# Optimization experiments

Hardware: AMD Instinct MI355X
Metric: run time of the kernel (lower is better)

Reference implementation:

```python
import jax, jax.numpy as jnp
import numpy as np


def setup_inputs() -> dict:
    key = jax.random.key(0)
    ks = jax.random.split(key, 8)
    bs, slen, d = 16, 2048, 1024
    scale = 1.0 / np.sqrt(d)
    return {
        "query": jax.random.normal(ks[0], (bs, d), jnp.float32),
        "states": jax.random.normal(ks[1], (bs, slen, d), jnp.float32),
        "Wq": jax.random.normal(ks[2], (d, d), jnp.float32) * scale,
        "bq": jax.random.normal(ks[3], (d,), jnp.float32) * 0.01,
        "Wk": jax.random.normal(ks[4], (d, d), jnp.float32) * scale,
        "bk": jax.random.normal(ks[5], (d,), jnp.float32) * 0.01,
        "We": jax.random.normal(ks[6], (2 * d,), jnp.float32) * scale,
        "be": jax.random.normal(ks[7], (1,), jnp.float32) * 0.01,
    }


def reference(query, states, Wq, bq, Wk, bk, We, be):
    d = Wq.shape[1]
    # q: (bs, d); k: (bs, slen, d)
    q = jax.nn.relu(query @ Wq + bq)
    k = jax.nn.relu(jnp.einsum("bsv,vd->bsd", states, Wk) + bk)
    # tanh(cat(q, k)) @ We == tanh(q) @ We[:d] + tanh(k) @ We[d:]
    # (avoids materializing the repeated/concatenated (bs, slen, 2d) tensor)
    We_q, We_k = We[:d], We[d:]
    energy = (jnp.tanh(q) @ We_q)[:, None] + jnp.einsum("bsd,d->bs", jnp.tanh(k), We_k) + be[0]
    attn_weights = jax.nn.softmax(energy, axis=1)  # (bs, slen)
    attn = jnp.einsum("bs,bsd->bd", attn_weights, states)  # weighted sum of values
    return attn_weights, attn
```

## Files before the change

### kernel.cpp

```cpp
#include <hip/hip_runtime.h>
#include <hip/hip_bf16.h>

#define D 1024
#define SLEN 2048
#define BS 16
#define MROWS (BS*SLEN)

typedef __attribute__((ext_vector_type(8))) short short8;
typedef __attribute__((ext_vector_type(4))) float f32x4;

__device__ __forceinline__ short f2bf(float f) {
  __hip_bfloat16 h = __float2bfloat16(f);
  return __builtin_bit_cast(short, h);
}

__device__ __forceinline__ float4 ntload4(const float* p) {
  f32x4 v = __builtin_nontemporal_load((const f32x4*)p);
  float4 r; r.x = v.x; r.y = v.y; r.z = v.z; r.w = v.w; return r;
}

__global__ __launch_bounds__(256) void wk_prep(const float* __restrict__ Wk,
                                               short* __restrict__ WkT) {
  const int g = blockIdx.x;
  const int t = threadIdx.x;
#pragma unroll
  for (int it = 0; it < 4; ++it) {
    const int n = it*256 + t;
    short8 p;
#pragma unroll
    for (int j = 0; j < 8; ++j)
      p[j] = f2bf(Wk[(size_t)(g*8 + j)*D + n]);
    *(short8*)(WkT + ((size_t)g*D + n)*8) = p;
  }
}

__global__ __launch_bounds__(512, 2) void energy_gemm(
    const float* __restrict__ states, const short* __restrict__ WkT,
    const float* __restrict__ bk, const float* __restrict__ We,
    float* __restrict__ eraw, float* __restrict__ attn)
{
  __shared__ short Al[64 * 129 * 8];

  const int tid  = threadIdx.x;
  const int w    = tid >> 6;
  const int lane = tid & 63;
  const int quad = lane >> 4;
  const int l16  = lane & 15;
  const int m0   = blockIdx.x * 64;

  if (blockIdx.x < BS && tid < 256) {
    f32x4 z = {0.f, 0.f, 0.f, 0.f};
    *(f32x4*)(attn + (size_t)blockIdx.x*D + tid*4) = z;
  }

  {
    const int row = tid >> 3;
    const int u0  = tid & 7;
    const float* Ag = states + (size_t)(m0 + row)*D;
#pragma unroll
    for (int i = 0; i < 16; ++i) {
      const int u = u0 + i*8;
      float4 x0 = ntload4(Ag + u*8);
      float4 x1 = ntload4(Ag + u*8 + 4);
      short8 p;
      p[0]=f2bf(x0.x); p[1]=f2bf(x0.y); p[2]=f2bf(x0.z); p[3]=f2bf(x0.w);
      p[4]=f2bf(x1.x); p[5]=f2bf(x1.y); p[6]=f2bf(x1.z); p[7]=f2bf(x1.w);
      *(short8*)(Al + ((size_t)row*129 + u)*8) = p;
    }
  }
  __syncthreads();

  f32x4 acc[2][4][4];
#pragma unroll
  for (int nc = 0; nc < 2; ++nc)
#pragma unroll
    for (int mi = 0; mi < 4; ++mi)
#pragma unroll
      for (int ni = 0; ni < 4; ++ni)
        acc[nc][mi][ni] = (f32x4){0.f, 0.f, 0.f, 0.f};

  const short* bbase = WkT + ((size_t)quad*D + w*128 + l16)*8;
  const short* abase = Al + ((size_t)l16*129 + quad)*8;

#define LOADB(ks, buf)                                                   \
  {                                                                      \
    const short* bp = bbase + (size_t)(ks)*32768;                        \
    _Pragma("unroll")                                                    \
    for (int nc = 0; nc < 2; ++nc)                                       \
      _Pragma("unroll")                                                  \
      for (int ni = 0; ni < 4; ++ni)                                     \
        buf[nc*4 + ni] = *(const short8*)(bp + nc*512 + ni*128);         \
  }

#define LOADA(ks, buf)                                                   \
  {                                                                      \
    _Pragma("unroll")                                                    \
    for (int mi = 0; mi < 4; ++mi)                                       \
      buf[mi] = *(const short8*)(abase + mi*16512 + (ks)*32);            \
  }

#define MFMAS(fa, fb)                                                    \
  {                                                                      \
    _Pragma("unroll")                                                    \
    for (int nc = 0; nc < 2; ++nc)                                       \
      _Pragma("unroll")                                                  \
      for (int mi = 0; mi < 4; ++mi)                                     \
        _Pragma("unroll")                                                \
        for (int ni = 0; ni < 4; ++ni)                                   \
          acc[nc][mi][ni] = __builtin_amdgcn_mfma_f32_16x16x32_bf16(     \
              fa[mi], fb[nc*4 + ni], acc[nc][mi][ni], 0, 0, 0);          \
  }

  short8 fa0[4], fa1[4], fb0[8], fb1[8];
  LOADA(0, fa0); LOADB(0, fb0);
#pragma unroll
  for (int kk = 0; kk < 16; ++kk) {
    LOADA(2*kk + 1, fa1); LOADB(2*kk + 1, fb1);
    MFMAS(fa0, fb0);
    if (kk < 15) { LOADA(2*kk + 2, fa0); LOADB(2*kk + 2, fb0); }
    MFMAS(fa1, fb1);
  }

  float esum[16];
#pragma unroll
  for (int q = 0; q < 16; ++q) esum[q] = 0.f;
#pragma unroll
  for (int nc = 0; nc < 2; ++nc)
#pragma unroll
    for (int ni = 0; ni < 4; ++ni) {
      const int n = w*128 + nc*64 + ni*16 + l16;
      const float bkv = bk[n];
      const float wev = We[D + n];
#pragma unroll
      for (int mi = 0; mi < 4; ++mi)
#pragma unroll
        for (int r = 0; r < 4; ++r) {
          float x = acc[nc][mi][ni][r] + bkv;
          x = fmaxf(x, 0.f);
          float ex = __expf(2.f * x);
          float th = 1.f - 2.f/(ex + 1.f);
          esum[mi*4 + r] += th * wev;
        }
    }
#pragma unroll
  for (int dd = 1; dd < 16; dd <<= 1)
#pragma unroll
    for (int q = 0; q < 16; ++q)
      esum[q] += __shfl_xor(esum[q], dd, 64);

  __syncthreads();
  float* red = (float*)Al;
  if (l16 == 0) {
#pragma unroll
    for (int mi = 0; mi < 4; ++mi)
#pragma unroll
      for (int r = 0; r < 4; ++r)
        red[(mi*16 + quad*4 + r)*8 + w] = esum[mi*4 + r];
  }
  __syncthreads();
  if (tid < 64) {
    float s = 0.f;
#pragma unroll
    for (int wi = 0; wi < 8; ++wi) s += red[tid*8 + wi];
    eraw[m0 + tid] = s;
  }
#undef LOADB
#undef LOADA
#undef MFMAS
}

__global__ __launch_bounds__(256) void softmax_w(
    const float* __restrict__ eraw, float* __restrict__ wts)
{
  const int b = blockIdx.x;
  const int t = threadIdx.x;
  __shared__ float red[256];

  float v[8];
  float m = -1e30f;
#pragma unroll
  for (int j = 0; j < 8; ++j) {
    v[j] = eraw[(size_t)b*SLEN + j*256 + t];
    m = fmaxf(m, v[j]);
  }
  red[t] = m; __syncthreads();
  for (int s = 128; s > 0; s >>= 1) {
    if (t < s) red[t] = fmaxf(red[t], red[t+s]);
    __syncthreads();
  }
  m = red[0];
  __syncthreads();

  float e[8];
  float sum = 0.f;
#pragma unroll
  for (int j = 0; j < 8; ++j) { e[j] = __expf(v[j] - m); sum += e[j]; }
  red[t] = sum; __syncthreads();
  for (int s = 128; s > 0; s >>= 1) {
    if (t < s) red[t] += red[t+s];
    __syncthreads();
  }
  const float inv = 1.f / red[0];
#pragma unroll
  for (int j = 0; j < 8; ++j)
    wts[(size_t)b*SLEN + j*256 + t] = e[j] * inv;
}

__global__ __launch_bounds__(512, 4) void attn_accum(
    const float* __restrict__ states, const float* __restrict__ wts,
    float* __restrict__ attn)
{
  const int sc = blockIdx.x;
  const int b  = blockIdx.y;
  const int t  = threadIdx.x;
  const int dq = (t & 255) << 2;
  const int ss = t >> 8;

  __shared__ float  wsh[64];
  __shared__ float4 part[256];

  if (t < 64) wsh[t] = wts[(size_t)b*SLEN + sc*64 + t];
  __syncthreads();

  const float* sp = states + ((size_t)b*SLEN + sc*64 + ss*32)*D + dq;
  float ax = 0.f, ay = 0.f, az = 0.f, aw = 0.f;
#pragma unroll
  for (int s = 0; s < 32; ++s) {
    float4 x = *(const float4*)(sp + (size_t)s*D);
    const float wv = wsh[ss*32 + s];
    ax = fmaf(wv, x.x, ax);
    ay = fmaf(wv, x.y, ay);
    az = fmaf(wv, x.z, az);
    aw = fmaf(wv, x.w, aw);
  }

  if (ss) part[t & 255] = (float4){ax, ay, az, aw};
  __syncthreads();
  if (!ss) {
    const float4 o = part[t];
    float* p = attn + (size_t)b*D + dq;
    atomicAdd(p + 0, ax + o.x);
    atomicAdd(p + 1, ay + o.y);
    atomicAdd(p + 2, az + o.z);
    atomicAdd(p + 3, aw + o.w);
  }
}

extern "C" void kernel_launch(void* const* d_in, const int* in_sizes, int n_in,
                              void* d_out, int out_size, void* d_ws, size_t ws_size,
                              hipStream_t stream) {
  const float* states = (const float*)d_in[1];
  const float* Wk     = (const float*)d_in[4];
  const float* bk     = (const float*)d_in[5];
  const float* We     = (const float*)d_in[6];
  float* out = (float*)d_out;

  short* WkT  = (short*)d_ws;
  float* eraw = (float*)((char*)d_ws + (size_t)D*D*sizeof(short));

  (void)in_sizes; (void)n_in; (void)out_size; (void)ws_size;

  wk_prep<<<128, 256, 0, stream>>>(Wk, WkT);
  energy_gemm<<<MROWS/64, 512, 0, stream>>>(states, WkT, bk, We, eraw, out + MROWS);
  softmax_w<<<BS, 256, 0, stream>>>(eraw, out);
  attn_accum<<<dim3(32, BS), 512, 0, stream>>>(states, out, out + MROWS);
}
```

Measured before the change: 301.7 us.

## Split GEMM N into two passes with triple-buffered B and fuse softmax into accumulation

The energy GEMM now handles its 128 output columns per wave in two passes of 64, halving the live accumulator registers. It triple-buffers the B fragments from global memory and raises wave priority around the MFMA groups. Softmax is folded into the attention accumulation kernel: each block recomputes the row max and sum from eraw with wave shuffles, which removes a launch but repeats the reduction in 32 blocks per batch. The two-pass split also reloads the A fragments from LDS twice.

```diff
diff --git a/kernel.cpp b/kernel.cpp
--- a/kernel.cpp
+++ b/kernel.cpp
@@ -70,26 +70,19 @@
   }
   __syncthreads();
 
-  f32x4 acc[2][4][4];
-#pragma unroll
-  for (int nc = 0; nc < 2; ++nc)
-#pragma unroll
-    for (int mi = 0; mi < 4; ++mi)
-#pragma unroll
-      for (int ni = 0; ni < 4; ++ni)
-        acc[nc][mi][ni] = (f32x4){0.f, 0.f, 0.f, 0.f};
-
   const short* bbase = WkT + ((size_t)quad*D + w*128 + l16)*8;
   const short* abase = Al + ((size_t)l16*129 + quad)*8;
 
-#define LOADB(ks, buf)                                                   \
+  float esum[16];
+#pragma unroll
+  for (int q = 0; q < 16; ++q) esum[q] = 0.f;
+
+#define LOADB3(ks, slot)                                                 \
   {                                                                      \
-    const short* bp = bbase + (size_t)(ks)*32768;                        \
+    const short* bp = bpass + (size_t)(ks)*32768;                        \
     _Pragma("unroll")                                                    \
-    for (int nc = 0; nc < 2; ++nc)                                       \
-      _Pragma("unroll")                                                  \
-      for (int ni = 0; ni < 4; ++ni)                                     \
-        buf[nc*4 + ni] = *(const short8*)(bp + nc*512 + ni*128);         \
+    for (int ni = 0; ni < 4; ++ni)                                       \
+      fb[slot][ni] = *(const short8*)(bp + ni*128);                      \
   }
 
 #define LOADA(ks, buf)                                                   \
@@ -99,49 +92,61 @@
       buf[mi] = *(const short8*)(abase + mi*16512 + (ks)*32);            \
   }
 
-#define MFMAS(fa, fb)                                                    \
+#define MFMAS16(fa, slot)                                                \
   {                                                                      \
+    __builtin_amdgcn_s_setprio(1);                                       \
     _Pragma("unroll")                                                    \
-    for (int nc = 0; nc < 2; ++nc)                                       \
+    for (int mi = 0; mi < 4; ++mi)                                       \
       _Pragma("unroll")                                                  \
-      for (int mi = 0; mi < 4; ++mi)                                     \
-        _Pragma("unroll")                                                \
-        for (int ni = 0; ni < 4; ++ni)                                   \
-          acc[nc][mi][ni] = __builtin_amdgcn_mfma_f32_16x16x32_bf16(     \
-              fa[mi], fb[nc*4 + ni], acc[nc][mi][ni], 0, 0, 0);          \
-  }
-
-  short8 fa0[4], fa1[4], fb0[8], fb1[8];
-  LOADA(0, fa0); LOADB(0, fb0);
-#pragma unroll
-  for (int kk = 0; kk < 16; ++kk) {
-    LOADA(2*kk + 1, fa1); LOADB(2*kk + 1, fb1);
-    MFMAS(fa0, fb0);
-    if (kk < 15) { LOADA(2*kk + 2, fa0); LOADB(2*kk + 2, fb0); }
-    MFMAS(fa1, fb1);
-  }
-
-  float esum[16];
-#pragma unroll
-  for (int q = 0; q < 16; ++q) esum[q] = 0.f;
-#pragma unroll
-  for (int nc = 0; nc < 2; ++nc)
+      for (int ni = 0; ni < 4; ++ni)                                     \
+        acc[mi][ni] = __builtin_amdgcn_mfma_f32_16x16x32_bf16(           \
+            fa[mi], fb[slot][ni], acc[mi][ni], 0, 0, 0);                 \
+    __builtin_amdgcn_s_setprio(0);                                       \
+  }
+
+#pragma unroll
+  for (int np = 0; np < 2; ++np) {
+    const short* bpass = bbase + np*512;
+
+    f32x4 acc[4][4];
+#pragma unroll
+    for (int mi = 0; mi < 4; ++mi)
+#pragma unroll
+      for (int ni = 0; ni < 4; ++ni)
+        acc[mi][ni] = (f32x4){0.f, 0.f, 0.f, 0.f};
+
+    short8 fb[3][4];
+    short8 fa0[4], fa1[4];
+    LOADB3(0, 0); LOADB3(1, 1); LOADB3(2, 2);
+    LOADA(0, fa0);
+#pragma unroll
+    for (int kk = 0; kk < 16; ++kk) {
+      LOADA(2*kk + 1, fa1);
+      MFMAS16(fa0, (2*kk) % 3);
+      if (2*kk + 3 < 32) LOADB3(2*kk + 3, (2*kk) % 3);
+      if (kk < 15) LOADA(2*kk + 2, fa0);
+      MFMAS16(fa1, (2*kk + 1) % 3);
+      if (2*kk + 4 < 32) LOADB3(2*kk + 4, (2*kk + 1) % 3);
+    }
+
 #pragma unroll
     for (int ni = 0; ni < 4; ++ni) {
-      const int n = w*128 + nc*64 + ni*16 + l16;
+      const int n = w*128 + np*64 + ni*16 + l16;
       const float bkv = bk[n];
       const float wev = We[D + n];
 #pragma unroll
       for (int mi = 0; mi < 4; ++mi)
 #pragma unroll
         for (int r = 0; r < 4; ++r) {
-          float x = acc[nc][mi][ni][r] + bkv;
+          float x = acc[mi][ni][r] + bkv;
           x = fmaxf(x, 0.f);
           float ex = __expf(2.f * x);
           float th = 1.f - 2.f/(ex + 1.f);
           esum[mi*4 + r] += th * wev;
         }
     }
+  }
+
 #pragma unroll
   for (int dd = 1; dd < 16; dd <<= 1)
 #pragma unroll
@@ -164,74 +169,72 @@
     for (int wi = 0; wi < 8; ++wi) s += red[tid*8 + wi];
     eraw[m0 + tid] = s;
   }
-#undef LOADB
+#undef LOADB3
 #undef LOADA
-#undef MFMAS
-}
-
-__global__ __launch_bounds__(256) void softmax_w(
-    const float* __restrict__ eraw, float* __restrict__ wts)
-{
-  const int b = blockIdx.x;
-  const int t = threadIdx.x;
-  __shared__ float red[256];
-
-  float v[8];
-  float m = -1e30f;
-#pragma unroll
-  for (int j = 0; j < 8; ++j) {
-    v[j] = eraw[(size_t)b*SLEN + j*256 + t];
-    m = fmaxf(m, v[j]);
-  }
-  red[t] = m; __syncthreads();
-  for (int s = 128; s > 0; s >>= 1) {
-    if (t < s) red[t] = fmaxf(red[t], red[t+s]);
-    __syncthreads();
-  }
-  m = red[0];
-  __syncthreads();
-
-  float e[8];
-  float sum = 0.f;
-#pragma unroll
-  for (int j = 0; j < 8; ++j) { e[j] = __expf(v[j] - m); sum += e[j]; }
-  red[t] = sum; __syncthreads();
-  for (int s = 128; s > 0; s >>= 1) {
-    if (t < s) red[t] += red[t+s];
-    __syncthreads();
-  }
-  const float inv = 1.f / red[0];
-#pragma unroll
-  for (int j = 0; j < 8; ++j)
-    wts[(size_t)b*SLEN + j*256 + t] = e[j] * inv;
-}
-
-__global__ __launch_bounds__(512, 4) void attn_accum(
-    const float* __restrict__ states, const float* __restrict__ wts,
-    float* __restrict__ attn)
+#undef MFMAS16
+}
+
+__global__ __launch_bounds__(512) void attn_fused(
+    const float* __restrict__ states, const float* __restrict__ eraw,
+    float* __restrict__ wts, float* __restrict__ attn)
 {
   const int sc = blockIdx.x;
   const int b  = blockIdx.y;
   const int t  = threadIdx.x;
+  const int wv = t >> 6;
+  const int lane = t & 63;
+
+  __shared__ float  redm[8];
+  __shared__ float  reds[8];
+  __shared__ float  wsh[64];
+  __shared__ float4 part[256];
+
+  float v[4];
+  float m = -1e30f;
+#pragma unroll
+  for (int j = 0; j < 4; ++j) {
+    v[j] = eraw[(size_t)b*SLEN + j*512 + t];
+    m = fmaxf(m, v[j]);
+  }
+#pragma unroll
+  for (int dd = 1; dd < 64; dd <<= 1) m = fmaxf(m, __shfl_xor(m, dd, 64));
+  if (lane == 0) redm[wv] = m;
+  __syncthreads();
+  float m2 = redm[0];
+#pragma unroll
+  for (int i = 1; i < 8; ++i) m2 = fmaxf(m2, redm[i]);
+
+  float sum = 0.f;
+#pragma unroll
+  for (int j = 0; j < 4; ++j) sum += __expf(v[j] - m2);
+#pragma unroll
+  for (int dd = 1; dd < 64; dd <<= 1) sum += __shfl_xor(sum, dd, 64);
+  if (lane == 0) reds[wv] = sum;
+  __syncthreads();
+  float s2 = 0.f;
+#pragma unroll
+  for (int i = 0; i < 8; ++i) s2 += reds[i];
+  const float inv = 1.f / s2;
+
+  if (t < 64) {
+    const float wvv = __expf(eraw[(size_t)b*SLEN + sc*64 + t] - m2) * inv;
+    wts[(size_t)b*SLEN + sc*64 + t] = wvv;
+    wsh[t] = wvv;
+  }
+  __syncthreads();
+
   const int dq = (t & 255) << 2;
   const int ss = t >> 8;
-
-  __shared__ float  wsh[64];
-  __shared__ float4 part[256];
-
-  if (t < 64) wsh[t] = wts[(size_t)b*SLEN + sc*64 + t];
-  __syncthreads();
-
   const float* sp = states + ((size_t)b*SLEN + sc*64 + ss*32)*D + dq;
   float ax = 0.f, ay = 0.f, az = 0.f, aw = 0.f;
 #pragma unroll
   for (int s = 0; s < 32; ++s) {
     float4 x = *(const float4*)(sp + (size_t)s*D);
-    const float wv = wsh[ss*32 + s];
-    ax = fmaf(wv, x.x, ax);
-    ay = fmaf(wv, x.y, ay);
-    az = fmaf(wv, x.z, az);
-    aw = fmaf(wv, x.w, aw);
+    const float wvv = wsh[ss*32 + s];
+    ax = fmaf(wvv, x.x, ax);
+    ay = fmaf(wvv, x.y, ay);
+    az = fmaf(wvv, x.z, az);
+    aw = fmaf(wvv, x.w, aw);
   }
 
   if (ss) part[t & 255] = (float4){ax, ay, az, aw};
@@ -262,6 +265,5 @@
 
   wk_prep<<<128, 256, 0, stream>>>(Wk, WkT);
   energy_gemm<<<MROWS/64, 512, 0, stream>>>(states, WkT, bk, We, eraw, out + MROWS);
-  softmax_w<<<BS, 256, 0, stream>>>(eraw, out);
-  attn_accum<<<dim3(32, BS), 512, 0, stream>>>(states, out, out + MROWS);
-}
+  attn_fused<<<dim3(32, BS), 512, 0, stream>>>(states, eraw, out, out + MROWS);
+}
```

After: 301.5 us. No clear change (-0.1%).
